# Kernel optimization log

Hardware: AMD Instinct MI355X
Metric: run time of the kernel (lower is better)

## Reference

```python
import jax, jax.numpy as jnp
import numpy as np

HID = 128

def setup_inputs() -> dict:
    key = jax.random.key(0)
    ks = jax.random.split(key, 16)
    T, N, E = 32, 10000, 160000
    features = jax.random.normal(ks[0], (T, N, 1), dtype=jnp.float32)
    src = jax.random.randint(ks[1], (E,), 0, N)
    dst = jax.random.randint(ks[2], (E,), 0, N)
    s = 0.1
    # GraphConv params (stored as [in,out] so y = x @ W + b)
    W1 = jax.random.normal(ks[3], (1, 32), dtype=jnp.float32) * s
    b1 = jnp.zeros((32,), jnp.float32)
    W2 = jax.random.normal(ks[4], (32, HID), dtype=jnp.float32) * s
    b2 = jnp.zeros((HID,), jnp.float32)
    # attention-pool gate nn.Linear(128,1)
    gate_w = jax.random.normal(ks[5], (HID, 1), dtype=jnp.float32) * s
    gate_b = jnp.zeros((1,), jnp.float32)
    # GRU params, PyTorch layout: [3H, in], gate order (r, z, n)
    W_ih = jax.random.normal(ks[6], (3 * HID, HID), dtype=jnp.float32) * s
    W_hh = jax.random.normal(ks[7], (3 * HID, HID), dtype=jnp.float32) * s
    b_ih = jnp.zeros((3 * HID,), jnp.float32)
    b_hh = jnp.zeros((3 * HID,), jnp.float32)
    # dense layers ([in,out])
    d1_w = jax.random.normal(ks[8], (HID, 16), dtype=jnp.float32) * s
    d1_b = jnp.zeros((16,), jnp.float32)
    d2_w = jax.random.normal(ks[9], (16, 4), dtype=jnp.float32) * s
    d2_b = jnp.zeros((4,), jnp.float32)
    return {"features": features, "src": src, "dst": dst,
            "W1": W1, "b1": b1, "W2": W2, "b2": b2,
            "gate_w": gate_w, "gate_b": gate_b,
            "W_ih": W_ih, "W_hh": W_hh, "b_ih": b_ih, "b_hh": b_hh,
            "d1_w": d1_w, "d1_b": d1_b, "d2_w": d2_w, "d2_b": d2_b}


def reference(features, src, dst, W1, b1, W2, b2, gate_w, gate_b,
              W_ih, W_hh, b_ih, b_hh, d1_w, d1_b, d2_w, d2_b):
    T, N, _ = features.shape
    E = src.shape[0]
    ones = jnp.ones((E,), features.dtype)
    out_deg = jnp.clip(jax.ops.segment_sum(ones, src, num_segments=N), 1.0)
    in_deg = jnp.clip(jax.ops.segment_sum(ones, dst, num_segments=N), 1.0)
    norm_out = out_deg ** -0.5  # DGL GraphConv norm='both' (src side)
    norm_in = in_deg ** -0.5    # dst side

    def gconv(h, W, b):
        # h: [N, F] -> scale by src norm, gather, scatter-add to dst, scale, linear, SiLU
        msg = (h * norm_out[:, None])[src]               # [E, F]
        agg = jax.ops.segment_sum(msg, dst, num_segments=N)  # [N, F]
        return jax.nn.silu((agg * norm_in[:, None]) @ W + b)

    def per_frame(f):  # f: [N,1]
        return gconv(gconv(f, W1, b1), W2, b2)  # [N, HID]

    h = jax.vmap(per_frame)(features)  # [T, N, HID]

    # GlobalAttentionPooling: softmax over nodes of gate_nn(h)
    gate = h @ gate_w + gate_b                 # [T, N, 1]
    alpha = jax.nn.softmax(gate, axis=1)
    pooled = jnp.sum(alpha * h, axis=1)        # [T, HID]

    # single-layer GRU, batch=1, take final hidden state
    def gru_step(hprev, x):
        gi = x @ W_ih.T + b_ih
        gh = hprev @ W_hh.T + b_hh
        i_r, i_z, i_n = jnp.split(gi, 3)
        h_r, h_z, h_n = jnp.split(gh, 3)
        r = jax.nn.sigmoid(i_r + h_r)
        z = jax.nn.sigmoid(i_z + h_z)
        n = jnp.tanh(i_n + r * h_n)
        hnew = (1.0 - z) * n + z * hprev
        return hnew, None

    h0 = jnp.zeros((HID,), features.dtype)
    hT, _ = jax.lax.scan(gru_step, h0, pooled)

    out = jax.nn.silu(hT @ d1_w + d1_b)
    out = jax.nn.silu(out @ d2_w + d2_b)
    return jax.nn.sigmoid(out).reshape(1, 4)
```

## Files before the change

### kernel.cpp

```cpp
#include <hip/hip_runtime.h>
#include <stdint.h>

#define T_FRAMES 32
#define NNODES 10000
#define NEDGES 160000
#define HID 128
#define LGX 32

#define H1_SCALE 512.0f
#define H1_INV   (1.0f/512.0f)

typedef short v8s __attribute__((ext_vector_type(8)));
typedef float v4f __attribute__((ext_vector_type(4)));

static __device__ __forceinline__ ushort f2bf(float f){
  uint32_t u = __float_as_uint(f);
  u += 0x7FFFu + ((u >> 16) & 1u);
  return (ushort)(u >> 16);
}
static __device__ __forceinline__ float fsigm(float x){
  return __fdividef(1.0f, 1.0f + __expf(-x));
}
static __device__ __forceinline__ float fsilu(float x){
  return x * fsigm(x);
}
static __device__ __forceinline__ float ftanh(float x){
  return 2.0f * fsigm(2.0f * x) - 1.0f;
}


__global__ void k_zero(float4* __restrict__ p, int n4){
  int i = blockIdx.x*blockDim.x + threadIdx.x;
  if (i < n4) p[i] = make_float4(0.f, 0.f, 0.f, 0.f);
}


__global__ void k_degree(const int* __restrict__ src, const int* __restrict__ dst,
                         int* cnt_out, int* cnt_in, int E){
  int e = blockIdx.x*blockDim.x + threadIdx.x;
  if (e < E){
    atomicAdd(&cnt_out[src[e]], 1);
    atomicAdd(&cnt_in[dst[e]], 1);
  }
}

__global__ void __launch_bounds__(1024) k_scan(const int* __restrict__ cnt_in,
                                               const int* __restrict__ cnt_out,
                                               int* row_ptr, int* cursor,
                                               float* norm_out, float* norm_in, int N){
  __shared__ int wsum[16];
  __shared__ int wexcl[16];
  int tid = threadIdx.x, lane = tid & 63, wid = tid >> 6;
  const int C = 10;
  int base = tid * C;
  int v[C];
  int s = 0;
  #pragma unroll
  for (int i = 0; i < C; ++i){
    int idx = base + i;
    int c = (idx < N) ? cnt_in[idx] : 0;
    v[i] = c;
    s += c;
    if (idx < N){
      norm_in[idx]  = rsqrtf((float)max(c, 1));
      norm_out[idx] = rsqrtf((float)max(cnt_out[idx], 1));
    }
  }
  int x = s;
  #pragma unroll
  for (int off = 1; off < 64; off <<= 1){
    int y = __shfl_up(x, off);
    if (lane >= off) x += y;
  }
  if (lane == 63) wsum[wid] = x;
  __syncthreads();
  if (tid == 0){
    int run = 0;
    #pragma unroll
    for (int w = 0; w < 16; ++w){ int t = wsum[w]; wexcl[w] = run; run += t; }
    row_ptr[N] = run;
  }
  __syncthreads();
  int run = wexcl[wid] + x - s;
  #pragma unroll
  for (int i = 0; i < C; ++i){
    int idx = base + i;
    if (idx < N){ row_ptr[idx] = run; cursor[idx] = run; run += v[i]; }
  }
}


__global__ void __launch_bounds__(256) k_fill_fnT(
    const int* __restrict__ src, const int* __restrict__ dst,
    int* cursor, int* es, int E,
    const float* __restrict__ feat, const float* __restrict__ norm_o,
    float* __restrict__ fnT,
    const float* __restrict__ W2, ushort* __restrict__ W2F, int N){
  __shared__ float sm[32][65];
  int tid = threadIdx.x;
  int bx = blockIdx.x;

  int e = bx*256 + tid;
  if (e < E){
    int p = atomicAdd(&cursor[dst[e]], 1);
    es[p] = src[e];
  }

  if (bx < 157){
    int n0 = bx*64;
    for (int idx = tid; idx < 2048; idx += 256){
      int t = idx >> 6, i = idx & 63;
      int n = n0 + i;
      sm[t][i] = (n < N) ? feat[(size_t)t*N + n] : 0.f;
    }
    __syncthreads();
    for (int idx = tid; idx < 2048; idx += 256){
      int i = idx >> 5, t = idx & 31;
      int n = n0 + i;
      if (n < N) fnT[(size_t)n*32 + t] = sm[t][i] * norm_o[n];
    }
  } else if (bx < 173){
    int t2 = (bx - 157)*256 + tid;
    int j = t2 & 7, l = (t2 >> 3) & 63, i = t2 >> 9;
    int g = l >> 4, n = l & 15;
    W2F[t2] = f2bf(W2[(g*8 + j)*128 + i*16 + n]);
  }
}


__global__ void __launch_bounds__(256) k_gconv1_nm(
    const float* __restrict__ fnT, const int* __restrict__ row_ptr,
    const int* __restrict__ es, const float* __restrict__ norm_in,
    const float* __restrict__ norm_out,
    const float* __restrict__ W1, const float* __restrict__ b1,
    uchar* __restrict__ h1s, int N){
  __shared__ float w1s[32], b1s[32];
  int tid = threadIdx.x;
  if (tid < 32){ w1s[tid] = W1[tid]; b1s[tid] = b1[tid]; }
  __syncthreads();
  int n = blockIdx.x*4 + (tid >> 6);
  int lane = tid & 63;
  int ep = lane >> 5, t = lane & 31;
  int s = row_ptr[n], d = row_ptr[n+1];
  float acc = 0.f;
  int e = s + ep;
  for (; e + 6 < d; e += 8){
    float v0 = fnT[(size_t)es[e]  *32 + t];
    float v1 = fnT[(size_t)es[e+2]*32 + t];
    float v2 = fnT[(size_t)es[e+4]*32 + t];
    float v3 = fnT[(size_t)es[e+6]*32 + t];
    acc += v0 + v1 + v2 + v3;
  }
  for (; e < d; e += 2)
    acc += fnT[(size_t)es[e]*32 + t];
  acc += __shfl_xor(acc, 32);
  float x1 = acc * norm_in[n];
  float x1p = __shfl(x1, lane >> 1);
  float no = norm_out[n];
  int j0 = (lane & 1) * 16;
  float hv[16];
  #pragma unroll
  for (int q = 0; q < 16; ++q)
    hv[q] = fsilu(fmaf(x1p, w1s[j0+q], b1s[j0+q])) * no;
  uint b[4] = {0u, 0u, 0u, 0u};
  #pragma unroll
  for (int q = 0; q < 16; ++q){
    float t8 = fminf(fmaxf(fmaf(hv[q], H1_SCALE, 128.5f), 0.f), 255.f);
    b[q >> 2] |= ((uint)(int)t8) << ((q & 3) * 8);
  }
  *(uint4*)(h1s + (size_t)n*1024 + lane*16) = make_uint4(b[0], b[1], b[2], b[3]);
}


__global__ void __launch_bounds__(256) k_gconv2_nm(
    const uchar* __restrict__ h1s, const int* __restrict__ row_ptr,
    const int* __restrict__ es, const float* __restrict__ norm_in,
    ushort* __restrict__ x2, int N){
  int tid = threadIdx.x;
  int n = blockIdx.x*4 + (tid >> 6);
  int lane = tid & 63;
  int s = row_ptr[n], d = row_ptr[n+1];
  float acc[16];
  #pragma unroll
  for (int i = 0; i < 16; ++i) acc[i] = 0.f;

  #define ACCB(v) do { \
    acc[0]  += (float)((v).x & 0xffu);         acc[1]  += (float)(((v).x >> 8) & 0xffu); \
    acc[2]  += (float)(((v).x >> 16) & 0xffu); acc[3]  += (float)((v).x >> 24); \
    acc[4]  += (float)((v).y & 0xffu);         acc[5]  += (float)(((v).y >> 8) & 0xffu); \
    acc[6]  += (float)(((v).y >> 16) & 0xffu); acc[7]  += (float)((v).y >> 24); \
    acc[8]  += (float)((v).z & 0xffu);         acc[9]  += (float)(((v).z >> 8) & 0xffu); \
    acc[10] += (float)(((v).z >> 16) & 0xffu); acc[11] += (float)((v).z >> 24); \
    acc[12] += (float)((v).w & 0xffu);         acc[13] += (float)(((v).w >> 8) & 0xffu); \
    acc[14] += (float)(((v).w >> 16) & 0xffu); acc[15] += (float)((v).w >> 24); \
  } while(0)

  int e = s;
  for (; e + 7 < d; e += 8){
    uint4 w0 = *((const uint4*)(h1s + (size_t)es[e]  *1024) + lane);
    uint4 w1 = *((const uint4*)(h1s + (size_t)es[e+1]*1024) + lane);
    uint4 w2 = *((const uint4*)(h1s + (size_t)es[e+2]*1024) + lane);
    uint4 w3 = *((const uint4*)(h1s + (size_t)es[e+3]*1024) + lane);
    uint4 w4 = *((const uint4*)(h1s + (size_t)es[e+4]*1024) + lane);
    uint4 w5 = *((const uint4*)(h1s + (size_t)es[e+5]*1024) + lane);
    uint4 w6 = *((const uint4*)(h1s + (size_t)es[e+6]*1024) + lane);
    uint4 w7 = *((const uint4*)(h1s + (size_t)es[e+7]*1024) + lane);
    ACCB(w0); ACCB(w1); ACCB(w2); ACCB(w3);
    ACCB(w4); ACCB(w5); ACCB(w6); ACCB(w7);
  }
  for (; e < d; ++e){
    uint4 w0 = *((const uint4*)(h1s + (size_t)es[e]*1024) + lane);
    ACCB(w0);
  }
  #undef ACCB

  float ni = norm_in[n];
  float corr = -128.0f * (float)(d - s);
  float sc = H1_INV * ni;
  uint w[8];
  #pragma unroll
  for (int q = 0; q < 8; ++q){
    float v0 = (acc[2*q]   + corr) * sc;
    float v1 = (acc[2*q+1] + corr) * sc;
    w[q] = (uint)f2bf(v0) | ((uint)f2bf(v1) << 16);
  }
  uint4* dp = (uint4*)(x2 + (size_t)n*1024 + lane*16);
  dp[0] = make_uint4(w[0], w[1], w[2], w[3]);
  dp[1] = make_uint4(w[4], w[5], w[6], w[7]);
}


__global__ void __launch_bounds__(256) k_linear_fused(
    const ushort* __restrict__ x2, const ushort* __restrict__ W2F,
    const float* __restrict__ b2, const float* __restrict__ gate_w,
    const float* __restrict__ gate_b,
    float* __restrict__ Zp, float* __restrict__ pooled_un, int N){
  __shared__ float pool_s[128];
  __shared__ float z_s[4];
  int t = blockIdx.y;
  int tid = threadIdx.x;
  int wave = tid >> 6, lane = tid & 63;
  int g = lane >> 4, n = lane & 15;
  if (tid < 128) pool_s[tid] = 0.f;
  if (tid < 4) z_s[tid] = 0.f;
  __syncthreads();

  const v8s* W2Fv = (const v8s*)W2F;
  v8s bfrag[8];
  #pragma unroll
  for (int i = 0; i < 8; ++i) bfrag[i] = W2Fv[i*64 + lane];
  float gw8[8], bv8[8];
  #pragma unroll
  for (int i = 0; i < 8; ++i){ gw8[i] = gate_w[i*16 + n]; bv8[i] = b2[i*16 + n]; }
  float gb = gate_b[0];

  float cs_acc[8];
  #pragma unroll
  for (int i = 0; i < 8; ++i) cs_acc[i] = 0.f;
  float z_acc = 0.f;

  int wslot = blockIdx.x*4 + wave;
  for (int tile = wslot; tile*16 < N; tile += 128){
    int nb = tile*16;
    const v8s* ap = (const v8s*)(x2 + (size_t)(nb + n)*1024 + t*32);
    v8s a = ap[g];
    v4f acc[8];
    #pragma unroll
    for (int i = 0; i < 8; ++i) acc[i] = (v4f){bv8[i], bv8[i], bv8[i], bv8[i]};
    #pragma unroll
    for (int i = 0; i < 8; ++i)
      acc[i] = __builtin_amdgcn_mfma_f32_16x16x32_bf16(a, bfrag[i], acc[i], 0, 0, 0);

    float hs[8][4];
    #pragma unroll
    for (int i = 0; i < 8; ++i){
      #pragma unroll
      for (int r = 0; r < 4; ++r) hs[i][r] = fsilu(acc[i][r]);
    }
    float gp[4] = {0.f, 0.f, 0.f, 0.f};
    #pragma unroll
    for (int i = 0; i < 8; ++i){
      #pragma unroll
      for (int r = 0; r < 4; ++r) gp[r] += hs[i][r] * gw8[i];
    }
    #pragma unroll
    for (int m = 1; m < 16; m <<= 1){
      #pragma unroll
      for (int r = 0; r < 4; ++r) gp[r] += __shfl_xor(gp[r], m);
    }
    float wn[4];
    #pragma unroll
    for (int r = 0; r < 4; ++r) wn[r] = __expf(gp[r] + gb);
    if (n == 0) z_acc += wn[0] + wn[1] + wn[2] + wn[3];
    #pragma unroll
    for (int i = 0; i < 8; ++i){
      #pragma unroll
      for (int r = 0; r < 4; ++r) cs_acc[i] += hs[i][r] * wn[r];
    }
  }

  z_acc += __shfl_xor(z_acc, 16);
  z_acc += __shfl_xor(z_acc, 32);
  if (lane == 0) z_s[wave] = z_acc;
  #pragma unroll
  for (int i = 0; i < 8; ++i){
    cs_acc[i] += __shfl_xor(cs_acc[i], 16);
    cs_acc[i] += __shfl_xor(cs_acc[i], 32);
  }
  if (lane < 16){
    #pragma unroll
    for (int i = 0; i < 8; ++i) atomicAdd(&pool_s[i*16 + lane], cs_acc[i]);
  }
  __syncthreads();
  if (tid == 0)
    Zp[(size_t)t*LGX + blockIdx.x] = z_s[0] + z_s[1] + z_s[2] + z_s[3];
  if (tid < 128) atomicAdd(&pooled_un[(size_t)t*HID + tid], pool_s[tid]);
}


__global__ void __launch_bounds__(768, 1) k_gru(
    const float* __restrict__ pooled_un, const float* __restrict__ Zp,
    const float* __restrict__ W_ih, const float* __restrict__ b_ih,
    const float* __restrict__ W_hh, const float* __restrict__ b_hh,
    const float* __restrict__ d1_w, const float* __restrict__ d1_b,
    const float* __restrict__ d2_w, const float* __restrict__ d2_b,
    float* __restrict__ out){
  __shared__ float tmp_i[768], tmp_h[768];
  __shared__ float ps_cur[HID], h_s[HID];
  __shared__ float invZ_s[T_FRAMES];
  __shared__ float o1[16];
  int tid = threadIdx.x;
  int half = (tid >= 384) ? 1 : 0;
  int o = tid - half*384;

  const float4* wih = (const float4*)(W_ih + (size_t)o*HID + half*64);
  const float4* whh = (const float4*)(W_hh + (size_t)o*HID + half*64);
  #define LDW(i) float4 WI##i = wih[i]; float4 WH##i = whh[i];
  LDW(0) LDW(1) LDW(2) LDW(3) LDW(4) LDW(5) LDW(6) LDW(7)
  LDW(8) LDW(9) LDW(10) LDW(11) LDW(12) LDW(13) LDW(14) LDW(15)
  #undef LDW
  float bi2 = half ? 0.f : b_ih[o];
  float bh2 = half ? 0.f : b_hh[o];

  if (tid < T_FRAMES){
    float z = 0.f;
    for (int i = 0; i < LGX; ++i) z += Zp[tid*LGX + i];
    invZ_s[tid] = __fdividef(1.0f, z);
  }
  if (tid < HID) h_s[tid] = 0.f;
  __syncthreads();

  for (int t = 0; t < T_FRAMES; ++t){
    if (tid < HID) ps_cur[tid] = pooled_un[(size_t)t*HID + tid] * invZ_s[t];
    __syncthreads();
    const float4* p4 = (const float4*)ps_cur + half*16;
    const float4* h4 = (const float4*)h_s + half*16;
    float ai = bi2, ah = bh2;
    #define STEP(i) { float4 pv = p4[i]; float4 hv = h4[i]; \
      ai = fmaf(WI##i.x, pv.x, ai); ai = fmaf(WI##i.y, pv.y, ai); \
      ai = fmaf(WI##i.z, pv.z, ai); ai = fmaf(WI##i.w, pv.w, ai); \
      ah = fmaf(WH##i.x, hv.x, ah); ah = fmaf(WH##i.y, hv.y, ah); \
      ah = fmaf(WH##i.z, hv.z, ah); ah = fmaf(WH##i.w, hv.w, ah); }
    STEP(0) STEP(1) STEP(2) STEP(3) STEP(4) STEP(5) STEP(6) STEP(7)
    STEP(8) STEP(9) STEP(10) STEP(11) STEP(12) STEP(13) STEP(14) STEP(15)
    #undef STEP
    tmp_i[tid] = ai;
    tmp_h[tid] = ah;
    __syncthreads();
    if (tid < HID){
      float gir = tmp_i[tid]       + tmp_i[384+tid];
      float giz = tmp_i[128+tid]   + tmp_i[512+tid];
      float gin = tmp_i[256+tid]   + tmp_i[640+tid];
      float ghr = tmp_h[tid]       + tmp_h[384+tid];
      float ghz = tmp_h[128+tid]   + tmp_h[512+tid];
      float ghn = tmp_h[256+tid]   + tmp_h[640+tid];
      float r  = fsigm(gir + ghr);
      float z  = fsigm(giz + ghz);
      float nn = ftanh(gin + r*ghn);
      h_s[tid] = (1.f - z)*nn + z*h_s[tid];
    }
    __syncthreads();
  }
  if (tid < 16){
    float acc = d1_b[tid];
    #pragma unroll 4
    for (int j = 0; j < HID; ++j) acc = fmaf(h_s[j], d1_w[j*16 + tid], acc);
    o1[tid] = fsilu(acc);
  }
  __syncthreads();
  if (tid < 4){
    float acc = d2_b[tid];
    #pragma unroll
    for (int j = 0; j < 16; ++j) acc = fmaf(o1[j], d2_w[j*4 + tid], acc);
    out[tid] = fsigm(fsilu(acc));
  }
}


extern "C" void kernel_launch(void* const* d_in, const int* in_sizes, int n_in,
                              void* d_out, int out_size, void* d_ws, size_t ws_size,
                              hipStream_t stream){
  const float* features = (const float*)d_in[0];
  const int*   src      = (const int*)  d_in[1];
  const int*   dst      = (const int*)  d_in[2];
  const float* W1       = (const float*)d_in[3];
  const float* b1       = (const float*)d_in[4];
  const float* W2       = (const float*)d_in[5];
  const float* b2       = (const float*)d_in[6];
  const float* gate_w   = (const float*)d_in[7];
  const float* gate_b   = (const float*)d_in[8];
  const float* W_ih     = (const float*)d_in[9];
  const float* W_hh     = (const float*)d_in[10];
  const float* b_ih     = (const float*)d_in[11];
  const float* b_hh     = (const float*)d_in[12];
  const float* d1_w     = (const float*)d_in[13];
  const float* d1_b     = (const float*)d_in[14];
  const float* d2_w     = (const float*)d_in[15];
  const float* d2_b     = (const float*)d_in[16];
  float* out = (float*)d_out;

  const int N = NNODES, E = NEDGES, T = T_FRAMES;

  char* base = (char*)d_ws;
  size_t off = 0;
  auto alloc = [&](size_t bytes)->void*{
    void* p = base + off;
    off = (off + bytes + 255) & ~(size_t)255;
    return p;
  };
  int*    cnt_out = (int*)   alloc((size_t)N*4);
  int*    cnt_in  = (int*)   alloc((size_t)N*4);
  float*  pooled  = (float*) alloc((size_t)T*HID*4);
  size_t zero_span = off;
  int*    row_ptr = (int*)   alloc((size_t)(N+1)*4);
  int*    cursor  = (int*)   alloc((size_t)N*4);
  float*  norm_o  = (float*) alloc((size_t)N*4);
  float*  norm_i  = (float*) alloc((size_t)N*4);
  int*    es      = (int*)   alloc((size_t)E*4);
  float*  fnT     = (float*) alloc((size_t)N*T*4);
  uchar*  h1s     = (uchar*) alloc((size_t)N*1024);
  ushort* x2      = (ushort*)alloc((size_t)N*T*32*2);
  float*  Zp      = (float*) alloc((size_t)T*LGX*4);
  ushort* W2F     = (ushort*)alloc((size_t)8*64*8*2);
  (void)ws_size; (void)in_sizes; (void)n_in; (void)out_size;

  int n4 = (int)(zero_span / 16);
  k_zero  <<<(n4+255)/256, 256, 0, stream>>>((float4*)d_ws, n4);

  k_degree<<<(E+255)/256, 256, 0, stream>>>(src, dst, cnt_out, cnt_in, E);
  k_scan  <<<1, 1024, 0, stream>>>(cnt_in, cnt_out, row_ptr, cursor, norm_o, norm_i, N);
  k_fill_fnT<<<(E+255)/256, 256, 0, stream>>>(src, dst, cursor, es, E,
                                              features, norm_o, fnT, W2, W2F, N);

  k_gconv1_nm<<<N/4, 256, 0, stream>>>(fnT, row_ptr, es, norm_i, norm_o, W1, b1, h1s, N);
  k_gconv2_nm<<<N/4, 256, 0, stream>>>(h1s, row_ptr, es, norm_i, x2, N);

  k_linear_fused<<<dim3(LGX, T), 256, 0, stream>>>(x2, W2F, b2, gate_w, gate_b, Zp, pooled, N);

  k_gru<<<1, 768, 0, stream>>>(pooled, Zp, W_ih, b_ih, W_hh, b_hh,
                               d1_w, d1_b, d2_w, d2_b, out);
}
```

Measured before the change: 189.8 us.

## Replace pooled atomics with per-block partials reduced inside GRU kernel

The fused linear kernel now writes per-block pooled partial sums to a workspace buffer instead of issuing global atomicAdds, so the pooled buffer no longer needs zeroing. The GRU kernel first reduces all partials into shared memory before the recurrence. It also keeps only W_hh in registers and reads W_ih from global/cache each step, dropping launch_bounds min-blocks to ease register pressure. The trade-off is extra serial reduction work in a single-block kernel and repeated W_ih loads on the sequential critical path.

```diff
diff --git a/kernel.cpp b/kernel.cpp
--- a/kernel.cpp
+++ b/kernel.cpp
@@ -234,7 +234,7 @@
     const ushort* __restrict__ x2, const ushort* __restrict__ W2F,
     const float* __restrict__ b2, const float* __restrict__ gate_w,
     const float* __restrict__ gate_b,
-    float* __restrict__ Zp, float* __restrict__ pooled_un, int N){
+    float* __restrict__ Zp, float* __restrict__ pool_part, int N){
   __shared__ float pool_s[128];
   __shared__ float z_s[4];
   int t = blockIdx.y;
@@ -314,51 +314,60 @@
   __syncthreads();
   if (tid == 0)
     Zp[(size_t)t*LGX + blockIdx.x] = z_s[0] + z_s[1] + z_s[2] + z_s[3];
-  if (tid < 128) atomicAdd(&pooled_un[(size_t)t*HID + tid], pool_s[tid]);
-}
-
-
-__global__ void __launch_bounds__(768, 1) k_gru(
-    const float* __restrict__ pooled_un, const float* __restrict__ Zp,
+  if (tid < 128)
+    pool_part[((size_t)t*LGX + blockIdx.x)*HID + tid] = pool_s[tid];
+}
+
+
+__global__ void __launch_bounds__(768) k_gru(
+    const float* __restrict__ pool_part, const float* __restrict__ Zp,
     const float* __restrict__ W_ih, const float* __restrict__ b_ih,
     const float* __restrict__ W_hh, const float* __restrict__ b_hh,
     const float* __restrict__ d1_w, const float* __restrict__ d1_b,
     const float* __restrict__ d2_w, const float* __restrict__ d2_b,
     float* __restrict__ out){
+  __shared__ float pooled_s[T_FRAMES][HID];
+  __shared__ float invZ_s[T_FRAMES];
+  __shared__ float ps_cur[HID], h_s[HID];
   __shared__ float tmp_i[768], tmp_h[768];
-  __shared__ float ps_cur[HID], h_s[HID];
-  __shared__ float invZ_s[T_FRAMES];
   __shared__ float o1[16];
   int tid = threadIdx.x;
   int half = (tid >= 384) ? 1 : 0;
   int o = tid - half*384;
 
-  const float4* wih = (const float4*)(W_ih + (size_t)o*HID + half*64);
-  const float4* whh = (const float4*)(W_hh + (size_t)o*HID + half*64);
-  #define LDW(i) float4 WI##i = wih[i]; float4 WH##i = whh[i];
-  LDW(0) LDW(1) LDW(2) LDW(3) LDW(4) LDW(5) LDW(6) LDW(7)
-  LDW(8) LDW(9) LDW(10) LDW(11) LDW(12) LDW(13) LDW(14) LDW(15)
-  #undef LDW
-  float bi2 = half ? 0.f : b_ih[o];
-  float bh2 = half ? 0.f : b_hh[o];
-
+  for (int idx = tid; idx < T_FRAMES*HID; idx += 768){
+    int t = idx >> 7, c = idx & 127;
+    float s = 0.f;
+    for (int b = 0; b < LGX; ++b) s += pool_part[((size_t)t*LGX + b)*HID + c];
+    pooled_s[t][c] = s;
+  }
   if (tid < T_FRAMES){
     float z = 0.f;
     for (int i = 0; i < LGX; ++i) z += Zp[tid*LGX + i];
     invZ_s[tid] = __fdividef(1.0f, z);
   }
+
+  const float4* whh = (const float4*)(W_hh + (size_t)o*HID + half*64);
+  #define LDW(i) float4 WH##i = whh[i];
+  LDW(0) LDW(1) LDW(2) LDW(3) LDW(4) LDW(5) LDW(6) LDW(7)
+  LDW(8) LDW(9) LDW(10) LDW(11) LDW(12) LDW(13) LDW(14) LDW(15)
+  #undef LDW
+  const float4* wih = (const float4*)(W_ih + (size_t)o*HID + half*64);
+  float bi2 = half ? 0.f : b_ih[o];
+  float bh2 = half ? 0.f : b_hh[o];
+
   if (tid < HID) h_s[tid] = 0.f;
   __syncthreads();
 
   for (int t = 0; t < T_FRAMES; ++t){
-    if (tid < HID) ps_cur[tid] = pooled_un[(size_t)t*HID + tid] * invZ_s[t];
+    if (tid < HID) ps_cur[tid] = pooled_s[t][tid] * invZ_s[t];
     __syncthreads();
     const float4* p4 = (const float4*)ps_cur + half*16;
     const float4* h4 = (const float4*)h_s + half*16;
     float ai = bi2, ah = bh2;
-    #define STEP(i) { float4 pv = p4[i]; float4 hv = h4[i]; \
-      ai = fmaf(WI##i.x, pv.x, ai); ai = fmaf(WI##i.y, pv.y, ai); \
-      ai = fmaf(WI##i.z, pv.z, ai); ai = fmaf(WI##i.w, pv.w, ai); \
+    #define STEP(i) { float4 wv = wih[i]; float4 pv = p4[i]; float4 hv = h4[i]; \
+      ai = fmaf(wv.x, pv.x, ai); ai = fmaf(wv.y, pv.y, ai); \
+      ai = fmaf(wv.z, pv.z, ai); ai = fmaf(wv.w, pv.w, ai); \
       ah = fmaf(WH##i.x, hv.x, ah); ah = fmaf(WH##i.y, hv.y, ah); \
       ah = fmaf(WH##i.z, hv.z, ah); ah = fmaf(WH##i.w, hv.w, ah); }
     STEP(0) STEP(1) STEP(2) STEP(3) STEP(4) STEP(5) STEP(6) STEP(7)
@@ -428,20 +437,20 @@
     off = (off + bytes + 255) & ~(size_t)255;
     return p;
   };
-  int*    cnt_out = (int*)   alloc((size_t)N*4);
-  int*    cnt_in  = (int*)   alloc((size_t)N*4);
-  float*  pooled  = (float*) alloc((size_t)T*HID*4);
+  int*    cnt_out  = (int*)   alloc((size_t)N*4);
+  int*    cnt_in   = (int*)   alloc((size_t)N*4);
   size_t zero_span = off;
-  int*    row_ptr = (int*)   alloc((size_t)(N+1)*4);
-  int*    cursor  = (int*)   alloc((size_t)N*4);
-  float*  norm_o  = (float*) alloc((size_t)N*4);
-  float*  norm_i  = (float*) alloc((size_t)N*4);
-  int*    es      = (int*)   alloc((size_t)E*4);
-  float*  fnT     = (float*) alloc((size_t)N*T*4);
-  uchar*  h1s     = (uchar*) alloc((size_t)N*1024);
-  ushort* x2      = (ushort*)alloc((size_t)N*T*32*2);
-  float*  Zp      = (float*) alloc((size_t)T*LGX*4);
-  ushort* W2F     = (ushort*)alloc((size_t)8*64*8*2);
+  int*    row_ptr  = (int*)   alloc((size_t)(N+1)*4);
+  int*    cursor   = (int*)   alloc((size_t)N*4);
+  float*  norm_o   = (float*) alloc((size_t)N*4);
+  float*  norm_i   = (float*) alloc((size_t)N*4);
+  int*    es       = (int*)   alloc((size_t)E*4);
+  float*  fnT      = (float*) alloc((size_t)N*T*4);
+  uchar*  h1s      = (uchar*) alloc((size_t)N*1024);
+  ushort* x2       = (ushort*)alloc((size_t)N*T*32*2);
+  float*  Zp       = (float*) alloc((size_t)T*LGX*4);
+  float*  pool_part= (float*) alloc((size_t)T*LGX*HID*4);
+  ushort* W2F      = (ushort*)alloc((size_t)8*64*8*2);
   (void)ws_size; (void)in_sizes; (void)n_in; (void)out_size;
 
   int n4 = (int)(zero_span / 16);
@@ -455,8 +464,8 @@
   k_gconv1_nm<<<N/4, 256, 0, stream>>>(fnT, row_ptr, es, norm_i, norm_o, W1, b1, h1s, N);
   k_gconv2_nm<<<N/4, 256, 0, stream>>>(h1s, row_ptr, es, norm_i, x2, N);
 
-  k_linear_fused<<<dim3(LGX, T), 256, 0, stream>>>(x2, W2F, b2, gate_w, gate_b, Zp, pooled, N);
-
-  k_gru<<<1, 768, 0, stream>>>(pooled, Zp, W_ih, b_ih, W_hh, b_hh,
+  k_linear_fused<<<dim3(LGX, T), 256, 0, stream>>>(x2, W2F, b2, gate_w, gate_b, Zp, pool_part, N);
+
+  k_gru<<<1, 768, 0, stream>>>(pool_part, Zp, W_ih, b_ih, W_hh, b_hh,
                                d1_w, d1_b, d2_w, d2_b, out);
 }
```

Result: no change. 189.3 us (-0.3%).
